# Optimization experiments

Measured on AMD Instinct MI355X. Metric: run time of the kernel, lower is better.

The kernel has to match this reference:

```python
import jax, jax.numpy as jnp
import numpy as np

HEADS = 8
DIM_HEAD = 128  # must equal the Triton BLOCK_N=128 for the kernel math to be well-defined
BLOCK_N = 128


def setup_inputs() -> dict:
    key = jax.random.key(0)
    k1, k2, k3 = jax.random.split(key, 3)
    B, S, D = 1, 2048, 1024
    dim_inner = HEADS * DIM_HEAD
    x = jax.random.normal(k1, (B, S, D), dtype=jnp.float32)
    w_qkv = jax.random.normal(k2, (D, 6 * dim_inner), dtype=jnp.float32) * 0.02
    w_out = jax.random.normal(k3, (dim_inner, D), dtype=jnp.float32) * 0.02
    return {"x": x, "w_qkv": w_qkv, "w_out": w_out}


def castle_attention(q, k, v, qu, ku, vu, scale):
    # q,k,v,qu,ku,vu: [b, h, s, d] with d == BLOCK_N (kernel constraint)
    b, h, s, d = q.shape
    q = q * scale
    qu = qu * scale
    qk = jnp.einsum('bhid,bhjd->bhij', q, k)      # [b,h,s,s]
    quku = jnp.einsum('bhid,bhjd->bhij', qu, ku)  # [b,h,s,s]
    i = jnp.arange(s)[:, None]
    j = jnp.arange(s)[None, :]
    causal = i >= j
    qk = jnp.where(causal, qk, -jnp.inf)
    # lookahead attention is sigmoid, zeroed on causal (non-strictly-future) positions
    la = jnp.where(causal, 0.0, jax.nn.sigmoid(quku))
    # per-key-block lookahead summary, exactly as the tiled Triton kernel computes it:
    # for key block t: su_t[m, :] = la[m, block_t] @ vu[block_t, :], then
    # scores[m, block_t] = qk[m, block_t] - silu(su_t[m, :])  (valid since d == BLOCK_N)
    nb = s // BLOCK_N
    la_b = la.reshape(b, h, s, nb, BLOCK_N)
    vu_b = vu.reshape(b, h, nb, BLOCK_N, d)
    su = jnp.einsum('bhmtc,bhtcd->bhmtd', la_b, vu_b)  # [b,h,s,nb,d], d == BLOCK_N
    scores = qk.reshape(b, h, s, nb, BLOCK_N) - jax.nn.silu(su)
    scores = scores.reshape(b, h, s, s)
    p = jax.nn.softmax(scores, axis=-1)
    return jnp.einsum('bhij,bhjd->bhid', p, v)


def reference(x, w_qkv, w_out):
    B, S, D = x.shape
    scale = DIM_HEAD ** -0.5
    qkvs = (x @ w_qkv).reshape(B, S, 6, HEADS, DIM_HEAD)
    qkvs = jnp.transpose(qkvs, (2, 0, 3, 1, 4))  # [6, b, h, s, d]
    qu, ku, vu, qc, kc, vc = (qkvs[t] for t in range(6))
    o = castle_attention(qc, kc, vc, qu, ku, vu, scale)  # [b,h,s,d]
    o = jnp.transpose(o, (0, 2, 1, 3)).reshape(B, S, HEADS * DIM_HEAD)
    return o @ w_out
```

## Files before the change

### kernel.cpp

```cpp
#include <hip/hip_runtime.h>

#define S_LEN 2048
#define DMODEL 1024
#define HEADS 8
#define DH 128
#define NQKV 6144
#define SCALE 0.08838834764831845f

typedef unsigned short u16;
typedef short s16x8 __attribute__((ext_vector_type(8)));
typedef short s16x4 __attribute__((ext_vector_type(4)));
typedef float f32x4 __attribute__((ext_vector_type(4)));

static __device__ __forceinline__ f32x4 mfma16(s16x8 a, s16x8 b, f32x4 c) {
  return __builtin_amdgcn_mfma_f32_16x16x32_bf16(a, b, c, 0, 0, 0);
}
static __device__ __forceinline__ u16 f2b(float f) {
  union { float f; unsigned u; } v; v.f = f;
  unsigned r = v.u + 0x7fffu + ((v.u >> 16) & 1u);
  return (u16)(r >> 16);
}
static __device__ __forceinline__ float b2f(u16 s) {
  union { unsigned u; float f; } v; v.u = ((unsigned)s) << 16;
  return v.f;
}
static __device__ __forceinline__ void gll16(const u16* g, u16* l) {
  __builtin_amdgcn_global_load_lds(
      (const __attribute__((address_space(1))) unsigned int*)g,
      (__attribute__((address_space(3))) unsigned int*)l, 16, 0, 0);
}

static __device__ const int SQB[60] = {
  0,1, 2,2, 3,3, 4,4,4, 5,5,5, 6,6,6, 7,7,7,7, 8,8,8,8, 9,9,9,9,
  10,10,10,10,10, 11,11,11,11,11, 12,12,12,12,12,
  13,13,13,13,13,13, 14,14,14,14,14,14, 15,15,15,15,15,15};
static __device__ const int ST0[60] = {
  0, 0, 0,2, 0,3, 0,2,4, 0,3,5, 0,3,6, 0,3,5,7, 0,3,6,8, 0,3,6,9,
  0,3,6,8,10, 0,3,6,9,11, 0,3,6,9,12,
  0,3,6,9,11,13, 0,3,6,9,12,14, 0,3,6,9,12,15};
static __device__ const int SNT[60] = {
  1, 2, 2,1, 3,1, 2,2,1, 3,2,1, 3,3,1, 3,2,2,1, 3,3,2,1, 3,3,3,1,
  3,3,2,2,1, 3,3,3,2,1, 3,3,3,3,1,
  3,3,3,2,2,1, 3,3,3,3,2,1, 3,3,3,3,3,1};
static __device__ const int S0T2[16] = {0,0,0,2,4,7,10,13,17,21,25,30,35,40,46,52};
static __device__ const int NCT2[16] = {0,0,2,2,3,3,3,4,4,4,5,5,5,6,6,6};

__global__ void __launch_bounds__(256)
k_prep(const float* __restrict__ x, const float* __restrict__ wqkv,
       const float* __restrict__ wout, u16* __restrict__ xb,
       u16* __restrict__ wqT, u16* __restrict__ woT) {
  const int bid = blockIdx.x, tid = threadIdx.x;
  if (bid < 2048) {
    int i = bid * 256 + tid;
    float4 v = reinterpret_cast<const float4*>(x)[i];
    s16x4 o;
    o[0] = (short)f2b(v.x); o[1] = (short)f2b(v.y);
    o[2] = (short)f2b(v.z); o[3] = (short)f2b(v.w);
    reinterpret_cast<s16x4*>(xb)[i] = o;
    return;
  }
  __shared__ float tile[64][65];
  const float* in;
  u16* out;
  int C, c0, r0;
  if (bid < 3584) {
    int j = bid - 2048;
    in = wqkv; out = wqT; C = NQKV;
    c0 = (j % 96) * 64; r0 = (j / 96) * 64;
  } else {
    int j = bid - 3584;
    in = wout; out = woT; C = DMODEL;
    c0 = (j & 15) * 64; r0 = (j >> 4) * 64;
  }
  const int rr = tid >> 4, cq = (tid & 15) * 4;
#pragma unroll
  for (int p = 0; p < 4; p++) {
    int r = rr + p * 16;
    float4 v = *reinterpret_cast<const float4*>(in + (size_t)(r0 + r) * C + c0 + cq);
    tile[r][cq] = v.x; tile[r][cq + 1] = v.y;
    tile[r][cq + 2] = v.z; tile[r][cq + 3] = v.w;
  }
  __syncthreads();
  const int cc = tid >> 3, rq = (tid & 7) * 8;
#pragma unroll
  for (int p = 0; p < 2; p++) {
    int c = cc + p * 32;
    s16x8 o;
#pragma unroll
    for (int jj = 0; jj < 8; jj++) o[jj] = (short)f2b(tile[rq + jj][c]);
    *reinterpret_cast<s16x8*>(out + (size_t)(c0 + c) * DMODEL + r0 + rq) = o;
  }
}

template <int MODE>
__global__ void __launch_bounds__(256, 3)
k_gemm2(const u16* __restrict__ A, const u16* __restrict__ Bt,
        u16* __restrict__ outb, float* __restrict__ outf) {
  const int tid = threadIdx.x;
  const int w = tid >> 6, l = tid & 63;
  const int lr = l & 15, lg = l >> 4;
  if (MODE == 0) {
    __shared__ u16 As[128 * 64];
    __shared__ u16 Bs[128 * 64];
    int m = blockIdx.x / 48, j = blockIdx.x % 48;
    int n = (j & 7) + 8 * (j >> 3);
    int m0 = m * 128, n0 = n * 128;
    const int wm = (w >> 1) * 64, wn = (w & 1) * 64;
    f32x4 acc[4][4] = {};
    for (int k0 = 0; k0 < DMODEL; k0 += 64) {
      __syncthreads();
#pragma unroll
      for (int jj = 0; jj < 8; jj++) {
        int c = w * 8 + jj;
        int cc = c & 15;
        int r = cc * 8 + (l >> 3);
        int s = l & 7;
        const u16* src = (c < 16 ? A + (size_t)(m0 + r) * DMODEL
                                 : Bt + (size_t)(n0 + r) * DMODEL)
                         + k0 + ((s ^ (r & 7)) * 8);
        gll16(src, (c < 16 ? As : Bs) + cc * 8 * 64);
      }
      asm volatile("s_waitcnt vmcnt(0)" ::: "memory");
      __syncthreads();
      s16x8 a[2][4], b[2][4];
#pragma unroll
      for (int hh = 0; hh < 2; hh++)
#pragma unroll
        for (int i = 0; i < 4; i++) {
          int ra = wm + i * 16 + lr;
          int oa = (ra * 128 + hh * 64 + lg * 16) ^ ((lr & 7) << 4);
          a[hh][i] = *reinterpret_cast<const s16x8*>((const char*)As + oa);
          int rb = wn + i * 16 + lr;
          int ob = (rb * 128 + hh * 64 + lg * 16) ^ ((lr & 7) << 4);
          b[hh][i] = *reinterpret_cast<const s16x8*>((const char*)Bs + ob);
        }
#pragma unroll
      for (int hh = 0; hh < 2; hh++)
#pragma unroll
        for (int i = 0; i < 4; i++)
#pragma unroll
          for (int jj = 0; jj < 4; jj++)
            acc[i][jj] = mfma16(a[hh][i], b[hh][jj], acc[i][jj]);
    }
    const int t = n >> 3, h = n & 7;
    u16* dst = outb + (size_t)(t * HEADS + h) * S_LEN * DH;
    if (t == 2 || t == 5) {
#pragma unroll
      for (int i = 0; i < 4; i++)
#pragma unroll
        for (int jj = 0; jj < 4; jj++) {
          int col = wn + jj * 16 + lr;
          int row0 = m0 + wm + i * 16 + lg * 4;
          s16x4 p;
#pragma unroll
          for (int e = 0; e < 4; e++) p[e] = (short)f2b(acc[i][jj][e]);
          *reinterpret_cast<s16x4*>(dst + (size_t)col * S_LEN + row0) = p;
        }
    } else {
      const float sc = (t == 0 || t == 3) ? SCALE : 1.0f;
#pragma unroll
      for (int i = 0; i < 4; i++)
#pragma unroll
        for (int jj = 0; jj < 4; jj++)
#pragma unroll
          for (int e = 0; e < 4; e++) {
            int row = m0 + wm + i * 16 + lg * 4 + e;
            int col = wn + jj * 16 + lr;
            dst[(size_t)row * DH + col] = f2b(acc[i][jj][e] * sc);
          }
    }
  } else {
    __shared__ u16 As[64 * 64];
    __shared__ u16 Bs[128 * 64];
    int m0 = blockIdx.y * 64, n0 = blockIdx.x * 128;
    const int wm = (w >> 1) * 32, wn = (w & 1) * 64;
    f32x4 acc[2][4] = {};
    for (int k0 = 0; k0 < DMODEL; k0 += 64) {
      __syncthreads();
#pragma unroll
      for (int jj = 0; jj < 8; jj++) {
        int c = w * 8 + jj;
        if (c < 24) {
          int isA = (c < 8);
          int cc = isA ? c : c - 8;
          int r = cc * 8 + (l >> 3);
          int s = l & 7;
          const u16* src = (isA ? A + (size_t)(m0 + r) * DMODEL
                                : Bt + (size_t)(n0 + r) * DMODEL)
                           + k0 + ((s ^ (r & 7)) * 8);
          gll16(src, (isA ? As : Bs) + cc * 8 * 64);
        }
      }
      asm volatile("s_waitcnt vmcnt(0)" ::: "memory");
      __syncthreads();
      s16x8 a[2][2], b[2][4];
#pragma unroll
      for (int hh = 0; hh < 2; hh++) {
#pragma unroll
        for (int i = 0; i < 2; i++) {
          int ra = wm + i * 16 + lr;
          int oa = (ra * 128 + hh * 64 + lg * 16) ^ ((lr & 7) << 4);
          a[hh][i] = *reinterpret_cast<const s16x8*>((const char*)As + oa);
        }
#pragma unroll
        for (int i = 0; i < 4; i++) {
          int rb = wn + i * 16 + lr;
          int ob = (rb * 128 + hh * 64 + lg * 16) ^ ((lr & 7) << 4);
          b[hh][i] = *reinterpret_cast<const s16x8*>((const char*)Bs + ob);
        }
      }
#pragma unroll
      for (int hh = 0; hh < 2; hh++)
#pragma unroll
        for (int i = 0; i < 2; i++)
#pragma unroll
          for (int jj = 0; jj < 4; jj++)
            acc[i][jj] = mfma16(a[hh][i], b[hh][jj], acc[i][jj]);
    }
#pragma unroll
    for (int i = 0; i < 2; i++)
#pragma unroll
      for (int jj = 0; jj < 4; jj++)
#pragma unroll
        for (int e = 0; e < 4; e++) {
          int row = m0 + wm + i * 16 + lg * 4 + e;
          int col = n0 + wn + jj * 16 + lr;
          outf[(size_t)row * DMODEL + col] = acc[i][jj][e];
        }
  }
}

__global__ void __launch_bounds__(512, 2)
k_attn1(const u16* __restrict__ qkvb, u16* __restrict__ op,
        float* __restrict__ ml, u16* __restrict__ obuf) {
  __shared__ u16 KA[128 * 128];
  __shared__ u16 VB[128 * 128];
  __shared__ u16 PB[128][42];
  const int h = blockIdx.x & 7, slot = blockIdx.x >> 3;
  const int qb = SQB[slot];
  const int t0 = ST0[slot];
  const int ntile = SNT[slot];
  const bool hasDiag = (t0 + ntile - 1 == qb);
  const int tid = threadIdx.x;
  const int w = tid >> 6, l = tid & 63;
  const int lr = l & 15, lg = l >> 4;
  const size_t hs = (size_t)S_LEN * DH;
  const u16* qu  = qkvb + (size_t)(0 * HEADS + h) * hs;
  const u16* ku  = qkvb + (size_t)(1 * HEADS + h) * hs;
  const u16* vuT = qkvb + (size_t)(2 * HEADS + h) * hs;
  const u16* qc  = qkvb + (size_t)(3 * HEADS + h) * hs;
  const u16* kc  = qkvb + (size_t)(4 * HEADS + h) * hs;
  const u16* vcT = qkvb + (size_t)(5 * HEADS + h) * hs;
  const int rq = qb * 128 + w * 16;

  f32x4 accO[8] = {};
  f32x4 accS[8];
  f32x4 corrF[8] = {};
  float mrun[4], lrun[4], fac[4];
#pragma unroll
  for (int e = 0; e < 4; e++) { mrun[e] = -INFINITY; lrun[e] = 0.f; }

  auto stageK = [&](const u16* kbase, int t) {
#pragma unroll
    for (int i = 0; i < 4; i++) {
      int r = w * 16 + i * 4 + (l >> 4);
      int s = l & 15;
      gll16(kbase + (size_t)t * 128 * DH + r * DH + ((s ^ (r & 15)) * 8),
            KA + (w * 16 + i * 4) * 128);
    }
  };
  auto stageV = [&](const u16* vbase, int t) {
#pragma unroll
    for (int i = 0; i < 4; i++) {
      int r = w * 16 + i * 4 + (l >> 4);
      int s = l & 15;
      gll16(vbase + (size_t)r * S_LEN + t * 128 + ((s ^ (r & 15)) * 8),
            VB + (w * 16 + i * 4) * 128);
    }
  };

  if (hasDiag) {
    stageK(ku, qb);
    stageV(vuT, qb);
    s16x8 aqu[4];
#pragma unroll
    for (int ks = 0; ks < 4; ks++)
      aqu[ks] = *reinterpret_cast<const s16x8*>(
          qu + (size_t)(rq + lr) * DH + ks * 32 + lg * 8);
    asm volatile("s_waitcnt vmcnt(4)" ::: "memory");
    __syncthreads();
    f32x4 s2[8] = {};
    __builtin_amdgcn_s_setprio(1);
#pragma unroll
    for (int ks = 0; ks < 4; ks++)
#pragma unroll
      for (int nf = 0; nf < 8; nf++) {
        int o = ((nf * 16 + lr) * 256 + ks * 64 + lg * 16) ^ (lr << 4);
        s16x8 b = *reinterpret_cast<const s16x8*>((const char*)KA + o);
        s2[nf] = mfma16(aqu[ks], b, s2[nf]);
      }
    __builtin_amdgcn_s_setprio(0);
    asm volatile("s_waitcnt vmcnt(0)" ::: "memory");
    __syncthreads();
#pragma unroll
    for (int qq = 0; qq < 4; qq++) {
#pragma unroll
      for (int jj = 0; jj < 2; jj++)
#pragma unroll
        for (int e = 0; e < 4; e++) {
          int rowq = w * 16 + lg * 4 + e;
          int col = (qq * 2 + jj) * 16 + lr;
          float x = s2[qq * 2 + jj][e];
          PB[w * 16 + lg * 4 + e][jj * 16 + lr] =
              f2b((col > rowq) ? 1.f / (1.f + __expf(-x)) : 0.f);
        }
      s16x8 p = *reinterpret_cast<const s16x8*>(&PB[w * 16 + lr][lg * 8]);
      __builtin_amdgcn_s_setprio(1);
#pragma unroll
      for (int nf = 0; nf < 8; nf++) {
        int o = ((nf * 16 + lr) * 256 + qq * 64 + lg * 16) ^ (lr << 4);
        s16x8 bv = *reinterpret_cast<const s16x8*>((const char*)VB + o);
        corrF[nf] = mfma16(p, bv, corrF[nf]);
      }
      __builtin_amdgcn_s_setprio(0);
    }
#pragma unroll
    for (int nf = 0; nf < 8; nf++)
#pragma unroll
      for (int e = 0; e < 4; e++) {
        float x = corrF[nf][e];
        corrF[nf][e] = x / (1.f + __expf(-x));
      }
    __syncthreads();
  }

  s16x8 aq[4];
#pragma unroll
  for (int ks = 0; ks < 4; ks++)
    aq[ks] = *reinterpret_cast<const s16x8*>(
        qc + (size_t)(rq + lr) * DH + ks * 32 + lg * 8);

  auto qkMfma = [&](bool dg) {
#pragma unroll
    for (int nf = 0; nf < 8; nf++) accS[nf] = f32x4{0.f, 0.f, 0.f, 0.f};
    __builtin_amdgcn_s_setprio(1);
#pragma unroll
    for (int ks = 0; ks < 4; ks++)
#pragma unroll
      for (int nf = 0; nf < 8; nf++) {
        int o = ((nf * 16 + lr) * 256 + ks * 64 + lg * 16) ^ (lr << 4);
        s16x8 b = *reinterpret_cast<const s16x8*>((const char*)KA + o);
        accS[nf] = mfma16(aq[ks], b, accS[nf]);
      }
    __builtin_amdgcn_s_setprio(0);
    if (dg) {
#pragma unroll
      for (int nf = 0; nf < 8; nf++)
#pragma unroll
        for (int e = 0; e < 4; e++) {
          int rowq = w * 16 + lg * 4 + e;
          int col = nf * 16 + lr;
          if (col > rowq) accS[nf][e] = -INFINITY;
          else accS[nf][e] -= corrF[nf][e];
        }
    }
#pragma unroll
    for (int e = 0; e < 4; e++) {
      float mx = accS[0][e];
#pragma unroll
      for (int nf = 1; nf < 8; nf++) mx = fmaxf(mx, accS[nf][e]);
#pragma unroll
      for (int off = 1; off < 16; off <<= 1) mx = fmaxf(mx, __shfl_xor(mx, off, 64));
      float mnew = fmaxf(mrun[e], mx);
      fac[e] = __expf(mrun[e] - mnew);
      mrun[e] = mnew;
#pragma unroll
      for (int nf = 0; nf < 8; nf++)
        accS[nf][e] = __expf(accS[nf][e] - mnew);
    }
  };
  auto smFinish = [&]() {
#pragma unroll
    for (int e = 0; e < 4; e++) {
      float rs = 0.f;
#pragma unroll
      for (int nf = 0; nf < 8; nf++) rs += accS[nf][e];
#pragma unroll
      for (int off = 1; off < 16; off <<= 1) rs += __shfl_xor(rs, off, 64);
      lrun[e] = lrun[e] * fac[e] + rs;
#pragma unroll
      for (int nf = 0; nf < 8; nf++) accO[nf][e] *= fac[e];
    }
  };
  auto pvTile = [&]() {
#pragma unroll
    for (int qq = 0; qq < 4; qq++) {
#pragma unroll
      for (int jj = 0; jj < 2; jj++)
#pragma unroll
        for (int e = 0; e < 4; e++)
          PB[w * 16 + lg * 4 + e][jj * 16 + lr] = f2b(accS[qq * 2 + jj][e]);
      s16x8 p = *reinterpret_cast<const s16x8*>(&PB[w * 16 + lr][lg * 8]);
      __builtin_amdgcn_s_setprio(1);
#pragma unroll
      for (int nf = 0; nf < 8; nf++) {
        int o = ((nf * 16 + lr) * 256 + qq * 64 + lg * 16) ^ (lr << 4);
        s16x8 bv = *reinterpret_cast<const s16x8*>((const char*)VB + o);
        accO[nf] = mfma16(p, bv, accO[nf]);
      }
      __builtin_amdgcn_s_setprio(0);
    }
  };

  stageK(kc, t0);
  stageV(vcT, t0);
  asm volatile("s_waitcnt vmcnt(4)" ::: "memory");
  __syncthreads();
  for (int i = 0; i < ntile; i++) {
    qkMfma(t0 + i == qb);
    asm volatile("s_waitcnt vmcnt(0)" ::: "memory");
    __syncthreads();
    if (i + 1 < ntile) stageK(kc, t0 + i + 1);
    smFinish();
    pvTile();
    asm volatile("s_waitcnt vmcnt(0)" ::: "memory");
    __syncthreads();
    if (i + 1 < ntile) stageV(vcT, t0 + i + 1);
  }

  if (slot < 2) {
#pragma unroll
    for (int nf = 0; nf < 8; nf++)
#pragma unroll
      for (int e = 0; e < 4; e++) {
        int row = w * 16 + lg * 4 + e;
        KA[row * 128 + nf * 16 + lr] = f2b(accO[nf][e] / lrun[e]);
      }
    __syncthreads();
#pragma unroll
    for (int i = 0; i < 4; i++) {
      int idx = tid + i * 512;
      int row = idx >> 4, c8 = (idx & 15) * 8;
      *reinterpret_cast<s16x8*>(obuf + (size_t)(qb * 128 + row) * DMODEL +
                                h * DH + c8) =
          reinterpret_cast<const s16x8*>(KA)[idx];
    }
  } else {
#pragma unroll
    for (int nf = 0; nf < 8; nf++)
#pragma unroll
      for (int e = 0; e < 4; e++) {
        int row = w * 16 + lg * 4 + e;
        KA[row * 128 + nf * 16 + lr] = f2b(accO[nf][e]);
      }
    __syncthreads();
    const int gs = h * 58 + slot - 2;
    u16* dst = op + (size_t)gs * 16384;
#pragma unroll
    for (int i = 0; i < 4; i++)
      reinterpret_cast<s16x8*>(dst)[tid + i * 512] =
          reinterpret_cast<const s16x8*>(KA)[tid + i * 512];
    if (lr == 0) {
      float* mlp = ml + (size_t)gs * 256;
#pragma unroll
      for (int e = 0; e < 4; e++) {
        int row = w * 16 + lg * 4 + e;
        mlp[row] = mrun[e];
        mlp[128 + row] = lrun[e];
      }
    }
  }
}

__global__ void __launch_bounds__(256)
k_attn2(const u16* __restrict__ op, const float* __restrict__ ml,
        u16* __restrict__ obuf) {
  const int h = blockIdx.x & 7, qb = 2 + (blockIdx.x >> 3);
  const int nc = NCT2[qb];
  const int base = h * 58 + S0T2[qb];
  const int row = threadIdx.x >> 1, c0 = (threadIdx.x & 1) * 64;
  float mg = -INFINITY;
  for (int c = 0; c < nc; c++) mg = fmaxf(mg, ml[(size_t)(base + c) * 256 + row]);
  float acc[64];
#pragma unroll
  for (int k = 0; k < 64; k++) acc[k] = 0.f;
  float lsum = 0.f;
  for (int c = 0; c < nc; c++) {
    int gs = base + c;
    const float* mlp = ml + (size_t)gs * 256;
    float f = __expf(mlp[row] - mg);
    lsum += f * mlp[128 + row];
    const u16* p = op + (size_t)gs * 16384 + row * 128 + c0;
#pragma unroll
    for (int k = 0; k < 8; k++) {
      s16x8 v = *reinterpret_cast<const s16x8*>(p + k * 8);
#pragma unroll
      for (int j = 0; j < 8; j++) acc[k * 8 + j] += f * b2f((u16)v[j]);
    }
  }
  float inv = 1.f / lsum;
  u16* dst = obuf + (size_t)(qb * 128 + row) * DMODEL + h * DH + c0;
#pragma unroll
  for (int k = 0; k < 8; k++) {
    s16x8 o;
#pragma unroll
    for (int j = 0; j < 8; j++) o[j] = (short)f2b(acc[k * 8 + j] * inv);
    *reinterpret_cast<s16x8*>(dst + k * 8) = o;
  }
}

extern "C" void kernel_launch(void* const* d_in, const int* in_sizes, int n_in,
                              void* d_out, int out_size, void* d_ws, size_t ws_size,
                              hipStream_t stream) {
  (void)in_sizes; (void)n_in; (void)out_size; (void)ws_size;
  const float* x = (const float*)d_in[0];
  const float* wqkv = (const float*)d_in[1];
  const float* wout = (const float*)d_in[2];
  char* ws = (char*)d_ws;
  u16* xb    = (u16*)(ws + 0);
  u16* wqT   = (u16*)(ws + 4194304);
  u16* opb   = (u16*)(ws + 0);
  float* mlb = (float*)(ws + 15990784);
  u16* woT   = (u16*)(ws + 16777216);
  u16* qkvb  = (u16*)(ws + 18874368);
  u16* obuf  = (u16*)(ws + 44040192);
  float* out = (float*)d_out;

  k_prep<<<3840, 256, 0, stream>>>(x, wqkv, wout, xb, wqT, woT);
  k_gemm2<0><<<768, 256, 0, stream>>>(xb, wqT, qkvb, nullptr);
  k_attn1<<<480, 512, 0, stream>>>(qkvb, opb, mlb, obuf);
  k_attn2<<<112, 256, 0, stream>>>(opb, mlb, obuf);
  k_gemm2<1><<<dim3(8, 32), 256, 0, stream>>>(obuf, woT, nullptr, out);
}
```

Baseline: 98.34 us.

## Fuse split-KV combine into attention kernel via last-block atomic counter

Removes the separate combine kernel by having each attention block atomically bump a per-(head, query-block) counter; the last block to finish merges all partial outputs using their stored max/sum statistics. It also repartitions the key tiles into 63 slots per head, with smaller chunks for mid-range query blocks, and places each slot's m/l stats right after its partial output. This saves a kernel launch and improves load balance, at the cost of threadfences, an atomic, and a serialized tail combine inside the last block. The counters live in the output buffer, which the final GEMM later overwrites.

Result: slower. 228.5 us (+132.3%).

```diff
diff --git a/kernel.cpp b/kernel.cpp
--- a/kernel.cpp
+++ b/kernel.cpp
@@ -30,27 +30,29 @@
       (__attribute__((address_space(3))) unsigned int*)l, 16, 0, 0);
 }
 
-static __device__ const int SQB[60] = {
-  0,1, 2,2, 3,3, 4,4,4, 5,5,5, 6,6,6, 7,7,7,7, 8,8,8,8, 9,9,9,9,
+static __device__ const int SQB[63] = {
+  0, 1, 2,2, 3,3,3, 4,4,4, 5,5,5,5, 6,6,6,6, 7,7,7,7, 8,8,8,8, 9,9,9,9,
   10,10,10,10,10, 11,11,11,11,11, 12,12,12,12,12,
   13,13,13,13,13,13, 14,14,14,14,14,14, 15,15,15,15,15,15};
-static __device__ const int ST0[60] = {
-  0, 0, 0,2, 0,3, 0,2,4, 0,3,5, 0,3,6, 0,3,5,7, 0,3,6,8, 0,3,6,9,
-  0,3,6,8,10, 0,3,6,9,11, 0,3,6,9,12,
-  0,3,6,9,11,13, 0,3,6,9,12,14, 0,3,6,9,12,15};
-static __device__ const int SNT[60] = {
-  1, 2, 2,1, 3,1, 2,2,1, 3,2,1, 3,3,1, 3,2,2,1, 3,3,2,1, 3,3,3,1,
-  3,3,2,2,1, 3,3,3,2,1, 3,3,3,3,1,
-  3,3,3,2,2,1, 3,3,3,3,2,1, 3,3,3,3,3,1};
-static __device__ const int S0T2[16] = {0,0,0,2,4,7,10,13,17,21,25,30,35,40,46,52};
-static __device__ const int NCT2[16] = {0,0,2,2,3,3,3,4,4,4,5,5,5,6,6,6};
+static __device__ const int ST0[63] = {
+  0, 0, 0,2, 0,2,3, 0,2,4, 0,2,4,5, 0,2,4,6, 0,3,6,7, 0,3,6,8, 0,3,6,9,
+  0,3,6,9,10, 0,3,6,9,11, 0,3,6,9,12,
+  0,3,6,9,12,13, 0,3,6,9,12,14, 0,3,6,9,12,15};
+static __device__ const int SNT[63] = {
+  1, 2, 2,1, 2,1,1, 2,2,1, 2,2,1,1, 2,2,2,1, 3,3,1,1, 3,3,2,1, 3,3,3,1,
+  3,3,3,1,1, 3,3,3,2,1, 3,3,3,3,1,
+  3,3,3,3,1,1, 3,3,3,3,2,1, 3,3,3,3,3,1};
+static __device__ const int NCT[16] = {1,1,2,3,3,4,4,4,4,4,5,5,5,6,6,6};
+static __device__ const int BST[16] = {0,0,0,2,5,8,12,16,20,24,28,33,38,43,49,55};
+#define SLOT_STRIDE 16896
 
 __global__ void __launch_bounds__(256)
 k_prep(const float* __restrict__ x, const float* __restrict__ wqkv,
        const float* __restrict__ wout, u16* __restrict__ xb,
-       u16* __restrict__ wqT, u16* __restrict__ woT) {
+       u16* __restrict__ wqT, u16* __restrict__ woT, int* __restrict__ ctr) {
   const int bid = blockIdx.x, tid = threadIdx.x;
   if (bid < 2048) {
+    if (bid == 0 && tid < 128) ctr[tid] = 0;
     int i = bid * 256 + tid;
     float4 v = reinterpret_cast<const float4*>(x)[i];
     s16x4 o;
@@ -232,10 +234,11 @@
 
 __global__ void __launch_bounds__(512, 2)
 k_attn1(const u16* __restrict__ qkvb, u16* __restrict__ op,
-        float* __restrict__ ml, u16* __restrict__ obuf) {
+        int* __restrict__ ctr, u16* __restrict__ obuf) {
   __shared__ u16 KA[128 * 128];
   __shared__ u16 VB[128 * 128];
   __shared__ u16 PB[128][42];
+  __shared__ int sOld;
   const int h = blockIdx.x & 7, slot = blockIdx.x >> 3;
   const int qb = SQB[slot];
   const int t0 = ST0[slot];
@@ -445,67 +448,69 @@
                                 h * DH + c8) =
           reinterpret_cast<const s16x8*>(KA)[idx];
     }
-  } else {
-#pragma unroll
-    for (int nf = 0; nf < 8; nf++)
-#pragma unroll
-      for (int e = 0; e < 4; e++) {
-        int row = w * 16 + lg * 4 + e;
-        KA[row * 128 + nf * 16 + lr] = f2b(accO[nf][e]);
-      }
-    __syncthreads();
-    const int gs = h * 58 + slot - 2;
-    u16* dst = op + (size_t)gs * 16384;
-#pragma unroll
-    for (int i = 0; i < 4; i++)
-      reinterpret_cast<s16x8*>(dst)[tid + i * 512] =
-          reinterpret_cast<const s16x8*>(KA)[tid + i * 512];
-    if (lr == 0) {
-      float* mlp = ml + (size_t)gs * 256;
-#pragma unroll
-      for (int e = 0; e < 4; e++) {
-        int row = w * 16 + lg * 4 + e;
-        mlp[row] = mrun[e];
-        mlp[128 + row] = lrun[e];
-      }
-    }
-  }
-}
-
-__global__ void __launch_bounds__(256)
-k_attn2(const u16* __restrict__ op, const float* __restrict__ ml,
-        u16* __restrict__ obuf) {
-  const int h = blockIdx.x & 7, qb = 2 + (blockIdx.x >> 3);
-  const int nc = NCT2[qb];
-  const int base = h * 58 + S0T2[qb];
-  const int row = threadIdx.x >> 1, c0 = (threadIdx.x & 1) * 64;
-  float mg = -INFINITY;
-  for (int c = 0; c < nc; c++) mg = fmaxf(mg, ml[(size_t)(base + c) * 256 + row]);
-  float acc[64];
-#pragma unroll
-  for (int k = 0; k < 64; k++) acc[k] = 0.f;
-  float lsum = 0.f;
-  for (int c = 0; c < nc; c++) {
-    int gs = base + c;
-    const float* mlp = ml + (size_t)gs * 256;
-    float f = __expf(mlp[row] - mg);
-    lsum += f * mlp[128 + row];
-    const u16* p = op + (size_t)gs * 16384 + row * 128 + c0;
-#pragma unroll
-    for (int k = 0; k < 8; k++) {
-      s16x8 v = *reinterpret_cast<const s16x8*>(p + k * 8);
-#pragma unroll
-      for (int j = 0; j < 8; j++) acc[k * 8 + j] += f * b2f((u16)v[j]);
-    }
-  }
-  float inv = 1.f / lsum;
-  u16* dst = obuf + (size_t)(qb * 128 + row) * DMODEL + h * DH + c0;
-#pragma unroll
-  for (int k = 0; k < 8; k++) {
-    s16x8 o;
-#pragma unroll
-    for (int j = 0; j < 8; j++) o[j] = (short)f2b(acc[k * 8 + j] * inv);
-    *reinterpret_cast<s16x8*>(dst + k * 8) = o;
+    return;
+  }
+#pragma unroll
+  for (int nf = 0; nf < 8; nf++)
+#pragma unroll
+    for (int e = 0; e < 4; e++) {
+      int row = w * 16 + lg * 4 + e;
+      KA[row * 128 + nf * 16 + lr] = f2b(accO[nf][e]);
+    }
+  __syncthreads();
+  const int gs = h * 61 + slot - 2;
+  u16* dst = op + (size_t)gs * SLOT_STRIDE;
+#pragma unroll
+  for (int i = 0; i < 4; i++)
+    reinterpret_cast<s16x8*>(dst)[tid + i * 512] =
+        reinterpret_cast<const s16x8*>(KA)[tid + i * 512];
+  if (lr == 0) {
+    float* mlp = (float*)(dst + 16384);
+#pragma unroll
+    for (int e = 0; e < 4; e++) {
+      int row = w * 16 + lg * 4 + e;
+      mlp[row] = mrun[e];
+      mlp[128 + row] = lrun[e];
+    }
+  }
+  __threadfence();
+  __syncthreads();
+  if (tid == 0) sOld = atomicAdd(ctr + h * 16 + qb, 1);
+  __syncthreads();
+  if (sOld == NCT[qb] - 1) {
+    __threadfence();
+    const int nc = NCT[qb];
+    const u16* base = op + (size_t)(h * 61 + BST[qb]) * SLOT_STRIDE;
+    const int r = tid >> 2, c0m = (tid & 3) * 32;
+    float mg = -INFINITY;
+    for (int c = 0; c < nc; c++)
+      mg = fmaxf(mg, ((const float*)(base + (size_t)c * SLOT_STRIDE + 16384))[r]);
+    float acc[32];
+#pragma unroll
+    for (int k = 0; k < 32; k++) acc[k] = 0.f;
+    float lsum = 0.f;
+    for (int c = 0; c < nc; c++) {
+      const u16* sp = base + (size_t)c * SLOT_STRIDE;
+      const float* mlp = (const float*)(sp + 16384);
+      float f = __expf(mlp[r] - mg);
+      lsum += f * mlp[128 + r];
+      const u16* p = sp + r * 128 + c0m;
+#pragma unroll
+      for (int k = 0; k < 4; k++) {
+        s16x8 v = *reinterpret_cast<const s16x8*>(p + k * 8);
+#pragma unroll
+        for (int jj = 0; jj < 8; jj++) acc[k * 8 + jj] += f * b2f((u16)v[jj]);
+      }
+    }
+    float inv = 1.f / lsum;
+    u16* dstO = obuf + (size_t)(qb * 128 + r) * DMODEL + h * DH + c0m;
+#pragma unroll
+    for (int k = 0; k < 4; k++) {
+      s16x8 o;
+#pragma unroll
+      for (int jj = 0; jj < 8; jj++) o[jj] = (short)f2b(acc[k * 8 + jj] * inv);
+      *reinterpret_cast<s16x8*>(dstO + k * 8) = o;
+    }
   }
 }
 
@@ -520,15 +525,14 @@
   u16* xb    = (u16*)(ws + 0);
   u16* wqT   = (u16*)(ws + 4194304);
   u16* opb   = (u16*)(ws + 0);
-  float* mlb = (float*)(ws + 15990784);
   u16* woT   = (u16*)(ws + 16777216);
   u16* qkvb  = (u16*)(ws + 18874368);
   u16* obuf  = (u16*)(ws + 44040192);
   float* out = (float*)d_out;
-
-  k_prep<<<3840, 256, 0, stream>>>(x, wqkv, wout, xb, wqT, woT);
+  int* ctr   = (int*)d_out;
+
+  k_prep<<<3840, 256, 0, stream>>>(x, wqkv, wout, xb, wqT, woT, ctr);
   k_gemm2<0><<<768, 256, 0, stream>>>(xb, wqT, qkvb, nullptr);
-  k_attn1<<<480, 512, 0, stream>>>(qkvb, opb, mlb, obuf);
-  k_attn2<<<112, 256, 0, stream>>>(opb, mlb, obuf);
+  k_attn1<<<504, 512, 0, stream>>>(qkvb, opb, ctr, obuf);
   k_gemm2<1><<<dim3(8, 32), 256, 0, stream>>>(obuf, woT, nullptr, out);
 }
```
